# Optimization experiments

Measured on AMD Instinct MI355X. Metric: run time of the kernel, lower is better.

Reference implementation:

```python
import jax, jax.numpy as jnp
import numpy as np

Q = 200000       # number of logical qubits
C = 64           # number of cores
D = 128          # core_emb_shape == d_E == d_H


def setup_inputs() -> dict:
    key = jax.random.key(0)
    k1, k2, k3, k4, k5, k6 = jax.random.split(key, 6)
    prev_assign = jax.random.randint(k1, (Q,), 0, C)
    q_embeddings = jax.random.normal(k2, (Q, D), dtype=jnp.float32)
    padding_emb = jnp.zeros((D,), dtype=jnp.float32)
    # symmetric 0/1 core connectivity matrix
    a = (jax.random.uniform(k3, (C, C)) < 0.3).astype(jnp.float32)
    core_con = jnp.maximum(a, a.T) * (1.0 - jnp.eye(C, dtype=jnp.float32))
    # single GNN layer params: relu(X Wself + A X Wmsg + b)
    W_self = jax.random.normal(k4, (D, D), dtype=jnp.float32) / np.sqrt(D)
    W_msg = jax.random.normal(k5, (D, D), dtype=jnp.float32) / np.sqrt(D)
    b = jax.random.normal(k6, (D,), dtype=jnp.float32) * 0.01
    return {"prev_assign": prev_assign, "q_embeddings": q_embeddings,
            "padding_emb": padding_emb, "core_con": core_con,
            "W_self": W_self, "W_msg": W_msg, "b": b}


def reference(prev_assign, q_embeddings, padding_emb, core_con, W_self, W_msg, b):
    n_cores = core_con.shape[0]
    # fused per-core max-reduce over qubit embeddings grouped by prev_assign
    seg_max = jax.ops.segment_max(q_embeddings, prev_assign, num_segments=n_cores)  # [C, D]
    counts = jax.ops.segment_sum(jnp.ones((q_embeddings.shape[0],), q_embeddings.dtype),
                                 prev_assign, num_segments=n_cores)                 # [C]
    core_embs = jnp.where((counts > 0)[:, None], seg_max, padding_emb[None, :])     # [C, D]
    # GNN over core connectivity graph (single message-passing layer)
    msg = core_con @ (core_embs @ W_msg)            # [C, D]
    return jax.nn.relu(core_embs @ W_self + msg + b)  # [C, D]
```

## Files before the change

### kernel.cpp

```cpp
#include <hip/hip_runtime.h>
#include <math.h>

#define D 128
#define C 64
#define P1_THREADS 256
#define P1_UNROLL 8

__global__ __launch_bounds__(P1_THREADS) void p1_segmax(
    const int* __restrict__ assign, const float* __restrict__ qe,
    float* __restrict__ part, int Q, int ntiles) {
  __shared__ float buf[2][C * D];
  int tid = threadIdx.x;
  float* flat = &buf[0][0];
  for (int i = tid; i < 2 * C * D; i += P1_THREADS) flat[i] = -INFINITY;
  __syncthreads();

  int p = tid >> 7;
  int t = tid & 127;
  float* mybuf = buf[p];

  for (int tile = blockIdx.x; tile < ntiles; tile += gridDim.x) {
    int base = tile * (2 * P1_UNROLL) + p * P1_UNROLL;
    if (base + P1_UNROLL <= Q) {
      float v[P1_UNROLL];
      int a[P1_UNROLL];
#pragma unroll
      for (int i = 0; i < P1_UNROLL; ++i) {
        v[i] = qe[(base + i) * D + t];
        a[i] = assign[base + i];
      }
#pragma unroll
      for (int i = 0; i < P1_UNROLL; ++i) {
        int idx = a[i] * D + t;
        mybuf[idx] = fmaxf(mybuf[idx], v[i]);
      }
    } else {
      for (int i = 0; i < P1_UNROLL; ++i) {
        int q = base + i;
        if (q < Q) {
          float v = qe[q * D + t];
          int idx = assign[q] * D + t;
          mybuf[idx] = fmaxf(mybuf[idx], v);
        }
      }
    }
  }
  __syncthreads();

  float* outp = part + (size_t)blockIdx.x * (C * D);
  for (int i = tid; i < C * D; i += P1_THREADS)
    outp[i] = fmaxf(buf[0][i], buf[1][i]);
}

__global__ __launch_bounds__(256) void p2_merge(
    const float* __restrict__ part, const float* __restrict__ padding,
    float* __restrict__ core_embs, int nb) {
  __shared__ float red[256];
  int tid = threadIdx.x;
  int o_local = tid & 15;
  int r = tid >> 4;
  int o = blockIdx.x * 16 + o_local;
  float m = -INFINITY;
  for (int br = r; br < nb; br += 16)
    m = fmaxf(m, part[(size_t)br * (C * D) + o]);
  red[tid] = m;
  __syncthreads();
  for (int s = 8; s >= 1; s >>= 1) {
    if (r < s)
      red[r * 16 + o_local] = fmaxf(red[r * 16 + o_local], red[(r + s) * 16 + o_local]);
    __syncthreads();
  }
  if (r == 0) {
    float v = red[o_local];
    if (v == -INFINITY) v = padding[o & (D - 1)];
    core_embs[o] = v;
  }
}

__global__ __launch_bounds__(D) void p3a_gemm(
    const float* __restrict__ core_embs, const float* __restrict__ Wmsg,
    float* __restrict__ tmp) {
  __shared__ float xrow[D];
  int t = threadIdx.x;
  int j = blockIdx.x;
  xrow[t] = core_embs[j * D + t];
  __syncthreads();
  float acc = 0.f;
#pragma unroll 8
  for (int k = 0; k < D; ++k) acc += xrow[k] * Wmsg[k * D + t];
  tmp[j * D + t] = acc;
}

__global__ __launch_bounds__(D) void p3b_out(
    const float* __restrict__ core_embs, const float* __restrict__ con,
    const float* __restrict__ tmp, const float* __restrict__ Wself,
    const float* __restrict__ b, float* __restrict__ out) {
  __shared__ float ce[D];
  __shared__ float cr[C];
  int t = threadIdx.x;
  int c = blockIdx.x;
  ce[t] = core_embs[c * D + t];
  if (t < C) cr[t] = con[c * C + t];
  __syncthreads();
  float acc = b[t];
#pragma unroll 8
  for (int k = 0; k < D; ++k) acc += ce[k] * Wself[k * D + t];
#pragma unroll 8
  for (int j = 0; j < C; ++j) acc += cr[j] * tmp[j * D + t];
  out[c * D + t] = fmaxf(acc, 0.f);
}

extern "C" void kernel_launch(void* const* d_in, const int* in_sizes, int n_in,
                              void* d_out, int out_size, void* d_ws, size_t ws_size,
                              hipStream_t stream) {
  const int* assign   = (const int*)d_in[0];
  const float* qe     = (const float*)d_in[1];
  const float* padding= (const float*)d_in[2];
  const float* con    = (const float*)d_in[3];
  const float* Wself  = (const float*)d_in[4];
  const float* Wmsg   = (const float*)d_in[5];
  const float* b      = (const float*)d_in[6];
  float* out = (float*)d_out;
  int Q = in_sizes[0];

  const size_t slot = (size_t)C * D;
  size_t avail_f = ws_size / sizeof(float);
  long nb_max = (long)((avail_f > 2 * slot ? avail_f - 2 * slot : slot) / slot);
  int nb = (int)(nb_max < 512 ? nb_max : 512);
  if (nb < 1) nb = 1;

  float* part      = (float*)d_ws;
  float* core_embs = part + (size_t)nb * slot;
  float* tmp       = core_embs + slot;

  int ntiles = (Q + 2 * P1_UNROLL - 1) / (2 * P1_UNROLL);

  hipLaunchKernelGGL(p1_segmax, dim3(nb), dim3(P1_THREADS), 0, stream,
                     assign, qe, part, Q, ntiles);
  hipLaunchKernelGGL(p2_merge, dim3((C * D) / 16), dim3(256), 0, stream,
                     part, padding, core_embs, nb);
  hipLaunchKernelGGL(p3a_gemm, dim3(C), dim3(D), 0, stream,
                     core_embs, Wmsg, tmp);
  hipLaunchKernelGGL(p3b_out, dim3(C), dim3(D), 0, stream,
                     core_embs, con, tmp, Wself, b, out);
}
```

Before: 190.4 us.

## Use order-preserving uint keys with LDS atomicMax and float4 loads in segmax

The per-block segment max now uses a single shared buffer of order-preserving unsigned keys updated with LDS atomicMax, replacing the two per-half float buffers updated with plain read-modify-write. Each warp lane loads a float4 per row, so a block covers 16 rows per iteration with wide loads. The shared layout is interleaved and transposed back on the final write, and the merge kernel reduces keys with integer max before decoding them to floats. Atomic contention in LDS and a different per-iteration access pattern are the trade-offs, and the old non-atomic RMW carried a race risk that the atomics remove.

```diff
diff --git a/kernel.cpp b/kernel.cpp
--- a/kernel.cpp
+++ b/kernel.cpp
@@ -4,76 +4,88 @@
 #define D 128
 #define C 64
 #define P1_THREADS 256
-#define P1_UNROLL 8
+#define P1_GRID 512
+
+__device__ __forceinline__ unsigned f2key(float f) {
+  unsigned u = __float_as_uint(f);
+  return (u & 0x80000000u) ? ~u : (u | 0x80000000u);
+}
+__device__ __forceinline__ float key2f(unsigned k) {
+  unsigned u = (k & 0x80000000u) ? (k & 0x7fffffffu) : ~k;
+  return __uint_as_float(u);
+}
 
 __global__ __launch_bounds__(P1_THREADS) void p1_segmax(
     const int* __restrict__ assign, const float* __restrict__ qe,
-    float* __restrict__ part, int Q, int ntiles) {
-  __shared__ float buf[2][C * D];
+    unsigned* __restrict__ part, int Q, int niter) {
+  __shared__ unsigned buf[C * D];
   int tid = threadIdx.x;
-  float* flat = &buf[0][0];
-  for (int i = tid; i < 2 * C * D; i += P1_THREADS) flat[i] = -INFINITY;
+  for (int i = tid; i < C * D; i += P1_THREADS) buf[i] = 0u;
   __syncthreads();
 
-  int p = tid >> 7;
-  int t = tid & 127;
-  float* mybuf = buf[p];
+  int lane = tid & 31;
+  int r = tid >> 5;
 
-  for (int tile = blockIdx.x; tile < ntiles; tile += gridDim.x) {
-    int base = tile * (2 * P1_UNROLL) + p * P1_UNROLL;
-    if (base + P1_UNROLL <= Q) {
-      float v[P1_UNROLL];
-      int a[P1_UNROLL];
-#pragma unroll
-      for (int i = 0; i < P1_UNROLL; ++i) {
-        v[i] = qe[(base + i) * D + t];
-        a[i] = assign[base + i];
-      }
-#pragma unroll
-      for (int i = 0; i < P1_UNROLL; ++i) {
-        int idx = a[i] * D + t;
-        mybuf[idx] = fmaxf(mybuf[idx], v[i]);
-      }
+  for (int it = blockIdx.x; it < niter; it += gridDim.x) {
+    int base = it * 16;
+    int r0 = base + r;
+    int r1 = base + 8 + r;
+    if (r1 < Q) {
+      float4 v0 = *(const float4*)&qe[(size_t)r0 * D + lane * 4];
+      float4 v1 = *(const float4*)&qe[(size_t)r1 * D + lane * 4];
+      int a0 = assign[r0] * D + lane;
+      int a1 = assign[r1] * D + lane;
+      atomicMax(&buf[a0 +  0], f2key(v0.x));
+      atomicMax(&buf[a0 + 32], f2key(v0.y));
+      atomicMax(&buf[a0 + 64], f2key(v0.z));
+      atomicMax(&buf[a0 + 96], f2key(v0.w));
+      atomicMax(&buf[a1 +  0], f2key(v1.x));
+      atomicMax(&buf[a1 + 32], f2key(v1.y));
+      atomicMax(&buf[a1 + 64], f2key(v1.z));
+      atomicMax(&buf[a1 + 96], f2key(v1.w));
     } else {
-      for (int i = 0; i < P1_UNROLL; ++i) {
-        int q = base + i;
-        if (q < Q) {
-          float v = qe[q * D + t];
-          int idx = assign[q] * D + t;
-          mybuf[idx] = fmaxf(mybuf[idx], v);
+      for (int rr = r0; rr <= base + 15; rr += 8) {
+        if (rr < Q) {
+          float4 v = *(const float4*)&qe[(size_t)rr * D + lane * 4];
+          int a = assign[rr] * D + lane;
+          atomicMax(&buf[a +  0], f2key(v.x));
+          atomicMax(&buf[a + 32], f2key(v.y));
+          atomicMax(&buf[a + 64], f2key(v.z));
+          atomicMax(&buf[a + 96], f2key(v.w));
         }
       }
     }
   }
   __syncthreads();
 
-  float* outp = part + (size_t)blockIdx.x * (C * D);
-  for (int i = tid; i < C * D; i += P1_THREADS)
-    outp[i] = fmaxf(buf[0][i], buf[1][i]);
+  unsigned* outp = part + (size_t)blockIdx.x * (C * D);
+  for (int i = tid; i < C * D; i += P1_THREADS) {
+    int c = i >> 7, d = i & 127;
+    outp[i] = buf[c * D + (d & 3) * 32 + (d >> 2)];
+  }
 }
 
 __global__ __launch_bounds__(256) void p2_merge(
-    const float* __restrict__ part, const float* __restrict__ padding,
+    const unsigned* __restrict__ part, const float* __restrict__ padding,
     float* __restrict__ core_embs, int nb) {
-  __shared__ float red[256];
+  __shared__ unsigned red[256];
   int tid = threadIdx.x;
   int o_local = tid & 15;
-  int r = tid >> 4;
+  int rdr = tid >> 4;
   int o = blockIdx.x * 16 + o_local;
-  float m = -INFINITY;
-  for (int br = r; br < nb; br += 16)
-    m = fmaxf(m, part[(size_t)br * (C * D) + o]);
+  unsigned m = 0u;
+  for (int br = rdr; br < nb; br += 16)
+    m = max(m, part[(size_t)br * (C * D) + o]);
   red[tid] = m;
   __syncthreads();
   for (int s = 8; s >= 1; s >>= 1) {
-    if (r < s)
-      red[r * 16 + o_local] = fmaxf(red[r * 16 + o_local], red[(r + s) * 16 + o_local]);
+    if (rdr < s)
+      red[rdr * 16 + o_local] = max(red[rdr * 16 + o_local], red[(rdr + s) * 16 + o_local]);
     __syncthreads();
   }
-  if (r == 0) {
-    float v = red[o_local];
-    if (v == -INFINITY) v = padding[o & (D - 1)];
-    core_embs[o] = v;
+  if (rdr == 0) {
+    unsigned k = red[o_local];
+    core_embs[o] = k ? key2f(k) : padding[o & (D - 1)];
   }
 }
 
@@ -113,30 +125,30 @@
 extern "C" void kernel_launch(void* const* d_in, const int* in_sizes, int n_in,
                               void* d_out, int out_size, void* d_ws, size_t ws_size,
                               hipStream_t stream) {
-  const int* assign   = (const int*)d_in[0];
-  const float* qe     = (const float*)d_in[1];
-  const float* padding= (const float*)d_in[2];
-  const float* con    = (const float*)d_in[3];
-  const float* Wself  = (const float*)d_in[4];
-  const float* Wmsg   = (const float*)d_in[5];
-  const float* b      = (const float*)d_in[6];
+  const int* assign    = (const int*)d_in[0];
+  const float* qe      = (const float*)d_in[1];
+  const float* padding = (const float*)d_in[2];
+  const float* con     = (const float*)d_in[3];
+  const float* Wself   = (const float*)d_in[4];
+  const float* Wmsg    = (const float*)d_in[5];
+  const float* b       = (const float*)d_in[6];
   float* out = (float*)d_out;
   int Q = in_sizes[0];
 
   const size_t slot = (size_t)C * D;
-  size_t avail_f = ws_size / sizeof(float);
-  long nb_max = (long)((avail_f > 2 * slot ? avail_f - 2 * slot : slot) / slot);
-  int nb = (int)(nb_max < 512 ? nb_max : 512);
+  size_t avail = ws_size / 4;
+  long nb_max = (long)((avail > 2 * slot ? avail - 2 * slot : slot) / slot);
+  int nb = (int)(nb_max < P1_GRID ? nb_max : P1_GRID);
   if (nb < 1) nb = 1;
 
-  float* part      = (float*)d_ws;
-  float* core_embs = part + (size_t)nb * slot;
+  unsigned* part   = (unsigned*)d_ws;
+  float* core_embs = (float*)((unsigned*)d_ws + (size_t)nb * slot);
   float* tmp       = core_embs + slot;
 
-  int ntiles = (Q + 2 * P1_UNROLL - 1) / (2 * P1_UNROLL);
+  int niter = (Q + 15) / 16;
 
   hipLaunchKernelGGL(p1_segmax, dim3(nb), dim3(P1_THREADS), 0, stream,
-                     assign, qe, part, Q, ntiles);
+                     assign, qe, part, Q, niter);
   hipLaunchKernelGGL(p2_merge, dim3((C * D) / 16), dim3(256), 0, stream,
                      part, padding, core_embs, nb);
   hipLaunchKernelGGL(p3a_gemm, dim3(C), dim3(D), 0, stream,
```

Result: slower. 196.4 us (+3.1%).
